# Kernel tuning notes

Hardware: AMD Instinct MI355X
Metric: run time of the kernel (lower is better)

The kernel has to match this reference:

```python
import jax, jax.numpy as jnp
import numpy as np

B, T, S = 4, 16, 4096
H, KV, D, DIM = 32, 8, 128, 4096
BASE = 10000.0
START = 2048
SCALE = 1.0 / np.sqrt(D)


def _rope(t, cos, sin):
    # t: [B, T, nh, D]; ggml 'normal' rope rotates adjacent pairs (x[2i], x[2i+1])
    b, tt, nh, d = t.shape
    t2 = t.reshape(b, tt, nh, d // 2, 2)
    x0, x1 = t2[..., 0], t2[..., 1]
    c = cos[None, :, None, :]  # [1, T, 1, D/2]
    s = sin[None, :, None, :]
    r = jnp.stack([x0 * c - x1 * s, x0 * s + x1 * c], axis=-1)
    return r.reshape(b, tt, nh, d)


def setup_inputs() -> dict:
    key = jax.random.key(0)
    ks = jax.random.split(key, 8)
    x = jax.random.normal(ks[0], (B, T, DIM), dtype=jnp.float32)
    k_cache = jax.random.normal(ks[1], (B, S, KV, D), dtype=jnp.float32)
    v_cache = jax.random.normal(ks[2], (B, S, KV, D), dtype=jnp.float32)
    wq = jax.random.normal(ks[3], (H * D, DIM), dtype=jnp.float32) * 0.02
    wk = jax.random.normal(ks[4], (KV * D, DIM), dtype=jnp.float32) * 0.02
    wv = jax.random.normal(ks[5], (KV * D, DIM), dtype=jnp.float32) * 0.02
    wo = jax.random.normal(ks[6], (DIM, H * D), dtype=jnp.float32) * 0.02
    input_pos = jnp.arange(T, dtype=jnp.int32) + START  # contiguous decode chunk
    inv_freq = BASE ** (-jnp.arange(0, D, 2, dtype=jnp.float32) / D)  # [D/2]
    ang = input_pos.astype(jnp.float32)[:, None] * inv_freq[None, :]  # [T, D/2]
    freqs_cos = jnp.cos(ang)
    freqs_sin = jnp.sin(ang)
    # causal mask: kv position <= query absolute position, [T, S] bool
    attn_mask = jnp.arange(S, dtype=jnp.int32)[None, :] <= input_pos[:, None]
    return {"x": x, "freqs_cos": freqs_cos, "freqs_sin": freqs_sin,
            "input_pos": input_pos, "attn_mask": attn_mask,
            "k_cache": k_cache, "v_cache": v_cache,
            "wq": wq, "wk": wk, "wv": wv, "wo": wo}


def reference(x, freqs_cos, freqs_sin, input_pos, attn_mask, k_cache, v_cache, wq, wk, wv, wo):
    b, t, _ = x.shape
    q = (x @ wq.T).reshape(b, t, H, D)
    k = (x @ wk.T).reshape(b, t, KV, D)
    v = (x @ wv.T).reshape(b, t, KV, D)
    q = _rope(q, freqs_cos, freqs_sin)
    k = _rope(k, freqs_cos, freqs_sin)
    # KV-cache scatter (index_copy_ along dim 1)
    kc = k_cache.at[:, input_pos].set(k)  # [B, S, KV, D]
    vc = v_cache.at[:, input_pos].set(v)
    g = H // KV
    qh = q.transpose(0, 2, 1, 3).reshape(b, KV, g, t, D)  # [B, KV, g, T, D]
    kf = kc.transpose(0, 2, 1, 3)  # [B, KV, S, D]
    vf = vc.transpose(0, 2, 1, 3)
    scores = jnp.einsum('bkgtd,bksd->bkgts', qh, kf) * SCALE
    scores = jnp.where(attn_mask[None, None, None], scores, jnp.finfo(scores.dtype).min)
    probs = jax.nn.softmax(scores, axis=-1)
    y = jnp.einsum('bkgts,bksd->bkgtd', probs, vf)  # [B, KV, g, T, D]
    y = y.reshape(b, H, t, D).transpose(0, 2, 1, 3).reshape(b, t, H * D)
    return y @ wo.T
```

## Files before the change

kernel.cpp:

```cpp
#include <hip/hip_runtime.h>
#include <hip/hip_bf16.h>


#define SCALE_F 0.08838834764831845f

typedef __attribute__((ext_vector_type(8))) short bf16x8;
typedef __attribute__((ext_vector_type(4))) float f32x4;

__device__ __forceinline__ unsigned short f2b(float f) {
    __hip_bfloat16 h = __float2bfloat16(f);
    return *reinterpret_cast<unsigned short*>(&h);
}

__device__ __forceinline__ bf16x8 pack8(float4 a, float4 b) {
    bf16x8 r;
    r[0] = (short)f2b(a.x); r[1] = (short)f2b(a.y); r[2] = (short)f2b(a.z); r[3] = (short)f2b(a.w);
    r[4] = (short)f2b(b.x); r[5] = (short)f2b(b.y); r[6] = (short)f2b(b.z); r[7] = (short)f2b(b.w);
    return r;
}

__device__ __forceinline__ void gl_lds16(const void* g, void* l) {
    __builtin_amdgcn_global_load_lds(
        (const __attribute__((address_space(1))) void*)g,
        (__attribute__((address_space(3))) void*)l, 16, 0, 0);
}


__global__ __launch_bounds__(256) void xcvt_kernel(
    const float* __restrict__ x, unsigned short* __restrict__ xb)
{
    const int flat = blockIdx.x * 256 + threadIdx.x;
    const int m = flat >> 9, rem = flat & 511;
    const int c = rem >> 2, j = rem & 3;
    const float* src = x + (size_t)m * 4096 + c * 32 + j * 8;
    float4 a = *(const float4*)src, b = *(const float4*)(src + 4);
    *(bf16x8*)(xb + c * 2048 + m * 32 + ((j ^ (m & 3)) * 8)) = pack8(a, b);
}

#define GEMM_BODY(WPTR, NN, LDW, APTR, CG_BASE, NCHUNK, ACC)                                   \
    const int l15 = lane & 15, lh = lane >> 4;                                                 \
    const int wr8 = lane >> 3, wc8 = lane & 7;                                                 \
    const float* wsrc = (WPTR) + (size_t)((NN) + 8 * wid + wr8) * (LDW)                        \
                      + ((wc8 ^ (wr8 & 7)) * 4);                                               \
    const unsigned short* asrc = (APTR) + (size_t)(CG_BASE) * 2048 + wid * 512 + lane * 8;     \
    float* wdst = &wlds[0][0] + wid * 256;                                \
    unsigned short* adst = &alds[0][0] + wid * 512;                     \
    _Pragma("unroll")                                                                          \
    for (int pc = 0; pc < 2; ++pc) {                                                           \
        gl_lds16(wsrc + (size_t)pc * 32, wdst + (size_t)pc * 1024);                            \
        gl_lds16(asrc + (size_t)pc * 2048, adst + (size_t)pc * 2048);                          \
    }                                                                                          \
    const int key = l15 & 7;                                                                   \
    const int akey = (l15 & 3);                                                                \
    for (int c = 0; c < (NCHUNK); ++c) {                                                       \
        if (c + 2 < (NCHUNK)) {                                                                \
            const int bq = (c + 2) & 3;                                                        \
            gl_lds16(wsrc + (size_t)(c + 2) * 32, wdst + (size_t)bq * 1024);                   \
            gl_lds16(asrc + (size_t)(c + 2) * 2048, adst + (size_t)bq * 2048);                 \
        }                                                                                      \
        if (c + 2 < (NCHUNK))      asm volatile("s_waitcnt vmcnt(4)" ::: "memory");            \
        else if (c + 1 < (NCHUNK)) asm volatile("s_waitcnt vmcnt(2)" ::: "memory");            \
        else                       asm volatile("s_waitcnt vmcnt(0)" ::: "memory");            \
        __builtin_amdgcn_s_barrier();                                                          \
        const int buf = c & 3;                                                                 \
        const float* wt = &wlds[buf][0];                                                       \
        const unsigned short* at = &alds[buf][0];                                              \
        const int arow = 16 * wid + l15;                                                       \
        bf16x8 a = *(const bf16x8*)(at + arow * 32 + ((lh ^ akey) * 8));                       \
        const float* w0p = wt + l15 * 32;                                                      \
        const float* w1p = wt + (16 + l15) * 32;                                               \
        const int c0 = ((2 * lh) ^ key) * 4, c1 = ((2 * lh + 1) ^ key) * 4;                    \
        bf16x8 b0 = pack8(*(const float4*)(w0p + c0), *(const float4*)(w0p + c1));             \
        bf16x8 b1 = pack8(*(const float4*)(w1p + c0), *(const float4*)(w1p + c1));             \
        ACC[0] = __builtin_amdgcn_mfma_f32_16x16x32_bf16(a, b0, ACC[0], 0, 0, 0);              \
        ACC[1] = __builtin_amdgcn_mfma_f32_16x16x32_bf16(a, b1, ACC[1], 0, 0, 0);              \
        __builtin_amdgcn_s_barrier();                                                          \
    }

__global__ __launch_bounds__(256) void qkv_gemm_kernel(
    const unsigned short* __restrict__ xb,
    const float* __restrict__ wq, const float* __restrict__ wk, const float* __restrict__ wvp,
    float* __restrict__ part)
{
    __shared__ float wlds[4][1024];
    __shared__ unsigned short alds[4][2048];
    const int tid = threadIdx.x, lane = tid & 63, wid = tid >> 6;
    const int n0 = blockIdx.x * 32;
    const int split = blockIdx.y;

    const float* wptr; int nn;
    if (n0 < 4096)      { wptr = wq;  nn = n0; }
    else if (n0 < 5120) { wptr = wk;  nn = n0 - 4096; }
    else                { wptr = wvp; nn = n0 - 5120; }

    f32x4 acc[2];
    acc[0] = (f32x4){0.f,0.f,0.f,0.f};
    acc[1] = (f32x4){0.f,0.f,0.f,0.f};

    const float* wbase = wptr + split * 512;
    GEMM_BODY(wbase, nn, 4096, xb, split * 16, 16, acc)

    float* pp = part + (size_t)split * 64 * 6144 + n0;
    #pragma unroll
    for (int nh = 0; nh < 2; ++nh)
        #pragma unroll
        for (int r = 0; r < 4; ++r)
            pp[(16 * wid + 4 * (lane >> 4) + r) * 6144 + nh * 16 + (lane & 15)] = acc[nh][r];
}

__global__ __launch_bounds__(256) void qkv_reduce_kernel(
    const float* __restrict__ part,
    const float* __restrict__ fcos, const float* __restrict__ fsin,
    unsigned short* __restrict__ q_out, unsigned short* __restrict__ k_new,
    unsigned short* __restrict__ v_new)
{
    const int gid = blockIdx.x * 256 + threadIdx.x;
    const int m = gid / 1536;
    const int n = (gid % 1536) * 4;
    float4 s = {0.f,0.f,0.f,0.f};
    #pragma unroll
    for (int sp = 0; sp < 8; ++sp) {
        float4 v = *(const float4*)(part + (size_t)(sp * 64 + m) * 6144 + n);
        s.x += v.x; s.y += v.y; s.z += v.z; s.w += v.w;
    }
    const int t = m & 15, b = m >> 4;
    ushort4 o;
    if (n < 5120) {
        int d = n & 127;
        float c0 = fcos[t * 64 + (d >> 1)],     s0 = fsin[t * 64 + (d >> 1)];
        float c1 = fcos[t * 64 + (d >> 1) + 1], s1 = fsin[t * 64 + (d >> 1) + 1];
        o.x = f2b(s.x * c0 - s.y * s0);
        o.y = f2b(s.x * s0 + s.y * c0);
        o.z = f2b(s.z * c1 - s.w * s1);
        o.w = f2b(s.z * s1 + s.w * c1);
    } else {
        o.x = f2b(s.x); o.y = f2b(s.y); o.z = f2b(s.z); o.w = f2b(s.w);
    }
    if (n < 4096) {
        int h = n >> 7, d = n & 127;
        int row = (b * 8 + (h >> 2)) * 64 + (h & 3) * 16 + t;
        *(ushort4*)(q_out + row * 128 + d) = o;
    } else if (n < 5120) {
        int idx = n - 4096, kvh = idx >> 7, d = idx & 127;
        *(ushort4*)(k_new + ((b * 8 + kvh) * 16 + t) * 128 + d) = o;
    } else {
        int idx = n - 5120, kvh = idx >> 7, d = idx & 127;
        *(ushort4*)(v_new + ((b * 8 + kvh) * 16 + t) * 128 + d) = o;
    }
}

__global__ __launch_bounds__(256) void attn_kernel(
    const float* __restrict__ k_cache, const float* __restrict__ v_cache,
    const unsigned short* __restrict__ q_glob,
    const unsigned short* __restrict__ k_new, const unsigned short* __restrict__ v_new,
    float* __restrict__ y_part, float* __restrict__ ml)
{
    __shared__ unsigned short smem[32256];
    unsigned short* kv_lds = smem;
    unsigned short* p_lds  = smem + 21504;

    const int bk = blockIdx.x >> 4;
    const int c  = blockIdx.x & 15;
    const int b = bk >> 3, kvh = bk & 7;
    const int tid = threadIdx.x, lane = tid & 63, wid = tid >> 6;
    const int s0 = c * 128;
    const bool last = (c == 15);

    bf16x8 aq[4];
    {
        const unsigned short* qp = q_glob + (bk * 64 + 16 * wid + (lane & 15)) * 128 + 8 * (lane >> 4);
        #pragma unroll
        for (int kk = 0; kk < 4; ++kk) aq[kk] = *(const bf16x8*)(qp + kk * 32);
    }

    const int rr = tid >> 5, ln4 = (tid & 31) * 4;
    {
        const float* kb = k_cache + ((size_t)(b * 4096 + s0) * 8 + kvh) * 128;
        #pragma unroll 4
        for (int it = 0; it < 16; ++it) {
            int srow = it * 8 + rr;
            float4 kf = *(const float4*)(kb + (size_t)srow * 1024 + ln4);
            ushort4 k4; k4.x = f2b(kf.x); k4.y = f2b(kf.y); k4.z = f2b(kf.z); k4.w = f2b(kf.w);
            *(ushort4*)&kv_lds[srow * 136 + ln4] = k4;
        }
        if (last) {
            int row = tid >> 4, c8 = (tid & 15) * 8;
            *(bf16x8*)&kv_lds[(128 + row) * 136 + c8] =
                *(const bf16x8*)(k_new + (bk * 16 + row) * 128 + c8);
        }
    }
    __syncthreads();

    f32x4 sc[9];
    f32x4 zero4 = {0.f,0.f,0.f,0.f};
    #pragma unroll
    for (int st = 0; st < 9; ++st) sc[st] = zero4;
    #pragma unroll
    for (int kk = 0; kk < 4; ++kk) {
        #pragma unroll
        for (int st = 0; st < 9; ++st) {
            if (st == 8 && !last) continue;
            bf16x8 bf = *(bf16x8*)&kv_lds[(st * 16 + (lane & 15)) * 136 + kk * 32 + 8 * (lane >> 4)];
            sc[st] = __builtin_amdgcn_mfma_f32_16x16x32_bf16(aq[kk], bf, sc[st], 0, 0, 0);
        }
    }

    float mrow[4], lrow[4];
    #pragma unroll
    for (int r = 0; r < 4; ++r) {
        int trow = 4 * (lane >> 4) + r;
        float mx = -3.0e38f;
        #pragma unroll
        for (int st = 0; st < 9; ++st) {
            if (st == 8 && !last) continue;
            float s = sc[st][r] * SCALE_F;
            if (st == 8 && (lane & 15) > trow) s = -3.0e38f;
            sc[st][r] = s;
            mx = fmaxf(mx, s);
        }
        mx = fmaxf(mx, __shfl_xor(mx, 1));
        mx = fmaxf(mx, __shfl_xor(mx, 2));
        mx = fmaxf(mx, __shfl_xor(mx, 4));
        mx = fmaxf(mx, __shfl_xor(mx, 8));
        float sum = 0.f;
        #pragma unroll
        for (int st = 0; st < 9; ++st) {
            if (st == 8 && !last) continue;
            float p = __expf(sc[st][r] - mx);
            sc[st][r] = p;
            sum += p;
        }
        sum += __shfl_xor(sum, 1);
        sum += __shfl_xor(sum, 2);
        sum += __shfl_xor(sum, 4);
        sum += __shfl_xor(sum, 8);
        mrow[r] = mx; lrow[r] = sum;
    }

    #pragma unroll
    for (int st = 0; st < 9; ++st) {
        if (st == 8 && !last) continue;
        #pragma unroll
        for (int r = 0; r < 4; ++r)
            p_lds[(16 * wid + 4 * (lane >> 4) + r) * 168 + st * 16 + (lane & 15)] = f2b(sc[st][r]);
    }
    if ((lane & 15) == 0) {
        #pragma unroll
        for (int r = 0; r < 4; ++r) {
            int row = 16 * wid + 4 * (lane >> 4) + r;
            ml[(bk * 16 + c) * 128 + row * 2 + 0] = mrow[r];
            ml[(bk * 16 + c) * 128 + row * 2 + 1] = lrow[r];
        }
    }
    __syncthreads();

    {
        const float* vb = v_cache + ((size_t)(b * 4096 + s0) * 8 + kvh) * 128;
        #pragma unroll 4
        for (int it = 0; it < 16; ++it) {
            int srow = it * 8 + rr;
            float4 vf = *(const float4*)(vb + (size_t)srow * 1024 + ln4);
            kv_lds[(ln4 + 0) * 168 + srow] = f2b(vf.x);
            kv_lds[(ln4 + 1) * 168 + srow] = f2b(vf.y);
            kv_lds[(ln4 + 2) * 168 + srow] = f2b(vf.z);
            kv_lds[(ln4 + 3) * 168 + srow] = f2b(vf.w);
        }
        if (last) {
            int row = tid >> 4, c8 = (tid & 15) * 8;
            bf16x8 vv = *(const bf16x8*)(v_new + (bk * 16 + row) * 128 + c8);
            #pragma unroll
            for (int u = 0; u < 8; ++u)
                kv_lds[(c8 + u) * 168 + 128 + row] = (unsigned short)vv[u];
            int pr = tid >> 2, pc = (tid & 3) * 4;
            #pragma unroll
            for (int u = 0; u < 4; ++u) p_lds[pr * 168 + 144 + pc + u] = 0;
            int vr = tid >> 1, vc = (tid & 1) * 8;
            #pragma unroll
            for (int u = 0; u < 8; ++u) kv_lds[vr * 168 + 144 + vc + u] = 0;
        }
    }
    __syncthreads();

    f32x4 o_[8];
    #pragma unroll
    for (int nt = 0; nt < 8; ++nt) o_[nt] = zero4;
    #pragma unroll
    for (int ks = 0; ks < 5; ++ks) {
        if (ks == 4 && !last) continue;
        bf16x8 a = *(bf16x8*)&p_lds[(16 * wid + (lane & 15)) * 168 + ks * 32 + 8 * (lane >> 4)];
        #pragma unroll
        for (int nt = 0; nt < 8; ++nt) {
            bf16x8 bf = *(bf16x8*)&kv_lds[(nt * 16 + (lane & 15)) * 168 + ks * 32 + 8 * (lane >> 4)];
            o_[nt] = __builtin_amdgcn_mfma_f32_16x16x32_bf16(a, bf, o_[nt], 0, 0, 0);
        }
    }
    float* yp = y_part + (size_t)(bk * 16 + c) * 8192;
    #pragma unroll
    for (int nt = 0; nt < 8; ++nt) {
        #pragma unroll
        for (int r = 0; r < 4; ++r)
            yp[(16 * wid + 4 * (lane >> 4) + r) * 128 + nt * 16 + (lane & 15)] = o_[nt][r];
    }
}

__global__ __launch_bounds__(256) void combine_kernel(
    const float* __restrict__ y_part, const float* __restrict__ ml,
    unsigned short* __restrict__ y_attn)
{
    const int bid = blockIdx.x;
    const int bk = bid >> 3, rg = bid & 7;
    const int b = bk >> 3, kvh = bk & 7;
    const int tid = threadIdx.x;
    const int d = tid & 127, r2 = tid >> 7;
    for (int rr = 0; rr < 8; rr += 2) {
        int row = rg * 8 + rr + r2;
        float mv[16], lv[16], M = -3.0e38f;
        #pragma unroll
        for (int cc = 0; cc < 16; ++cc) {
            mv[cc] = ml[(bk * 16 + cc) * 128 + row * 2 + 0];
            lv[cc] = ml[(bk * 16 + cc) * 128 + row * 2 + 1];
            M = fmaxf(M, mv[cc]);
        }
        float den = 0.f, acc = 0.f;
        #pragma unroll
        for (int cc = 0; cc < 16; ++cc) {
            float co = __expf(mv[cc] - M);
            den += co * lv[cc];
            acc += co * y_part[((size_t)(bk * 16 + cc) * 64 + row) * 128 + d];
        }
        float y = acc / den;
        int gi = row >> 4, t = row & 15;
        int m = b * 16 + t;
        int n = (kvh * 4 + gi) * 128 + d;
        int c = n >> 5, j = (n >> 3) & 3, lo = n & 7;
        y_attn[c * 2048 + m * 32 + ((j ^ (m & 3)) * 8) + lo] = f2b(y);
    }
}

__global__ __launch_bounds__(256) void proj_gemm_kernel(
    const unsigned short* __restrict__ y_attn, const float* __restrict__ wo,
    float* __restrict__ part)
{
    __shared__ float wlds[4][1024];
    __shared__ unsigned short alds[4][2048];
    const int tid = threadIdx.x, lane = tid & 63, wid = tid >> 6;
    const int n0 = blockIdx.x * 32;
    const int split = blockIdx.y;

    f32x4 acc[2];
    acc[0] = (f32x4){0.f,0.f,0.f,0.f};
    acc[1] = (f32x4){0.f,0.f,0.f,0.f};

    const float* wbase = wo + split * 512;
    GEMM_BODY(wbase, n0, 4096, y_attn, split * 16, 16, acc)

    float* pp = part + (size_t)split * 64 * 4096 + n0;
    #pragma unroll
    for (int nh = 0; nh < 2; ++nh)
        #pragma unroll
        for (int r = 0; r < 4; ++r)
            pp[(16 * wid + 4 * (lane >> 4) + r) * 4096 + nh * 16 + (lane & 15)] = acc[nh][r];
}

__global__ __launch_bounds__(256) void proj_reduce_kernel(
    const float* __restrict__ part, float* __restrict__ out)
{
    const int gid = blockIdx.x * 256 + threadIdx.x;
    const int m = gid >> 10;
    const int n = (gid & 1023) * 4;
    float4 s = {0.f,0.f,0.f,0.f};
    #pragma unroll
    for (int sp = 0; sp < 8; ++sp) {
        float4 v = *(const float4*)(part + (size_t)(sp * 64 + m) * 4096 + n);
        s.x += v.x; s.y += v.y; s.z += v.z; s.w += v.w;
    }
    *(float4*)(out + (size_t)m * 4096 + n) = s;
}

extern "C" void kernel_launch(void* const* d_in, const int* in_sizes, int n_in,
                              void* d_out, int out_size, void* d_ws, size_t ws_size,
                              hipStream_t stream)
{
    const float* x       = (const float*)d_in[0];
    const float* fcos    = (const float*)d_in[1];
    const float* fsin    = (const float*)d_in[2];
    const float* k_cache = (const float*)d_in[5];
    const float* v_cache = (const float*)d_in[6];
    const float* wq      = (const float*)d_in[7];
    const float* wk      = (const float*)d_in[8];
    const float* wv      = (const float*)d_in[9];
    const float* wo      = (const float*)d_in[10];

    char* p = (char*)d_ws;
    unsigned short* q_out  = (unsigned short*)p; p += 4 * 8 * 64 * 128 * 2;
    unsigned short* k_new  = (unsigned short*)p; p += 4 * 8 * 16 * 128 * 2;
    unsigned short* v_new  = (unsigned short*)p; p += 4 * 8 * 16 * 128 * 2;
    unsigned short* y_attn = (unsigned short*)p; p += 64 * 4096 * 2;
    unsigned short* x_bf16 = (unsigned short*)p; p += 64 * 4096 * 2;
    float* mlbuf  = (float*)p; p += 32 * 16 * 64 * 2 * 4;
    float* y_part = (float*)p; p += (size_t)32 * 16 * 64 * 128 * 4;
    float* bigbuf = (float*)p;

    xcvt_kernel<<<128, 256, 0, stream>>>(x, x_bf16);
    qkv_gemm_kernel<<<dim3(192, 8), 256, 0, stream>>>(x_bf16, wq, wk, wv, bigbuf);
    qkv_reduce_kernel<<<384, 256, 0, stream>>>(bigbuf, fcos, fsin, q_out, k_new, v_new);
    attn_kernel<<<512, 256, 0, stream>>>(k_cache, v_cache, q_out, k_new, v_new, y_part, mlbuf);
    combine_kernel<<<256, 256, 0, stream>>>(y_part, mlbuf, y_attn);
    proj_gemm_kernel<<<dim3(128, 8), 256, 0, stream>>>(y_attn, wo, bigbuf);
    proj_reduce_kernel<<<256, 256, 0, stream>>>(bigbuf, (float*)d_out);
}
```

Baseline: 85.65 us.

## Retile QKV and output GEMMs to 256-wide N tiles with 16-way split-K

Both weight GEMMs now give each block a 256-column N tile, with each wave computing a 64x64 register tile (4x4 MFMA fragments) instead of a 32-column tile. The K dimension is split 16 ways rather than 8, and the reduce kernels sum 16 partials. Pipelining drops from four buffers to double buffering with larger chunks. The aim is to reuse each loaded A fragment across more MFMAs and cut per-block overhead, at the cost of far fewer blocks (384 and 256), more partial-sum traffic, and higher register and LDS use.

```diff
diff --git a/kernel.cpp b/kernel.cpp
--- a/kernel.cpp
+++ b/kernel.cpp
@@ -37,43 +37,43 @@
     *(bf16x8*)(xb + c * 2048 + m * 32 + ((j ^ (m & 3)) * 8)) = pack8(a, b);
 }
 
-#define GEMM_BODY(WPTR, NN, LDW, APTR, CG_BASE, NCHUNK, ACC)                                   \
+#define GEMM_TILE(WLANE, ASRC, NC, ACC)                                                        \
     const int l15 = lane & 15, lh = lane >> 4;                                                 \
-    const int wr8 = lane >> 3, wc8 = lane & 7;                                                 \
-    const float* wsrc = (WPTR) + (size_t)((NN) + 8 * wid + wr8) * (LDW)                        \
-                      + ((wc8 ^ (wr8 & 7)) * 4);                                               \
-    const unsigned short* asrc = (APTR) + (size_t)(CG_BASE) * 2048 + wid * 512 + lane * 8;     \
-    float* wdst = &wlds[0][0] + wid * 256;                                \
-    unsigned short* adst = &alds[0][0] + wid * 512;                     \
+    float* wd0 = &wlds[0][0] + wid * 2048;                                                     \
+    unsigned short* ad0 = &alds[0][0] + wid * 512;                                             \
     _Pragma("unroll")                                                                          \
-    for (int pc = 0; pc < 2; ++pc) {                                                           \
-        gl_lds16(wsrc + (size_t)pc * 32, wdst + (size_t)pc * 1024);                            \
-        gl_lds16(asrc + (size_t)pc * 2048, adst + (size_t)pc * 2048);                          \
-    }                                                                                          \
-    const int key = l15 & 7;                                                                   \
-    const int akey = (l15 & 3);                                                                \
-    for (int c = 0; c < (NCHUNK); ++c) {                                                       \
-        if (c + 2 < (NCHUNK)) {                                                                \
-            const int bq = (c + 2) & 3;                                                        \
-            gl_lds16(wsrc + (size_t)(c + 2) * 32, wdst + (size_t)bq * 1024);                   \
-            gl_lds16(asrc + (size_t)(c + 2) * 2048, adst + (size_t)bq * 2048);                 \
+    for (int i = 0; i < 8; ++i) gl_lds16((WLANE) + (size_t)i * 8 * 4096, wd0 + i * 256);       \
+    gl_lds16((ASRC), ad0);                                                                     \
+    for (int c = 0; c < (NC); ++c) {                                                           \
+        if (c + 1 < (NC)) {                                                                    \
+            const int bq = (c + 1) & 1;                                                        \
+            float* wd = &wlds[0][0] + bq * 8192 + wid * 2048;                                  \
+            unsigned short* ad = &alds[0][0] + bq * 2048 + wid * 512;                          \
+            _Pragma("unroll")                                                                  \
+            for (int i = 0; i < 8; ++i)                                                        \
+                gl_lds16((WLANE) + (size_t)i * 8 * 4096 + (c + 1) * 32, wd + i * 256);         \
+            gl_lds16((ASRC) + (size_t)(c + 1) * 2048, ad);                                     \
+            asm volatile("s_waitcnt vmcnt(9)" ::: "memory");                                   \
+        } else {                                                                               \
+            asm volatile("s_waitcnt vmcnt(0)" ::: "memory");                                   \
         }                                                                                      \
-        if (c + 2 < (NCHUNK))      asm volatile("s_waitcnt vmcnt(4)" ::: "memory");            \
-        else if (c + 1 < (NCHUNK)) asm volatile("s_waitcnt vmcnt(2)" ::: "memory");            \
-        else                       asm volatile("s_waitcnt vmcnt(0)" ::: "memory");            \
         __builtin_amdgcn_s_barrier();                                                          \
-        const int buf = c & 3;                                                                 \
-        const float* wt = &wlds[buf][0];                                                       \
-        const unsigned short* at = &alds[buf][0];                                              \
-        const int arow = 16 * wid + l15;                                                       \
-        bf16x8 a = *(const bf16x8*)(at + arow * 32 + ((lh ^ akey) * 8));                       \
-        const float* w0p = wt + l15 * 32;                                                      \
-        const float* w1p = wt + (16 + l15) * 32;                                               \
-        const int c0 = ((2 * lh) ^ key) * 4, c1 = ((2 * lh + 1) ^ key) * 4;                    \
-        bf16x8 b0 = pack8(*(const float4*)(w0p + c0), *(const float4*)(w0p + c1));             \
-        bf16x8 b1 = pack8(*(const float4*)(w1p + c0), *(const float4*)(w1p + c1));             \
-        ACC[0] = __builtin_amdgcn_mfma_f32_16x16x32_bf16(a, b0, ACC[0], 0, 0, 0);              \
-        ACC[1] = __builtin_amdgcn_mfma_f32_16x16x32_bf16(a, b1, ACC[1], 0, 0, 0);              \
+        const int buf = c & 1;                                                                 \
+        const unsigned short* at = &alds[0][0] + buf * 2048;                                   \
+        const float* wt = &wlds[0][0] + buf * 8192;                                            \
+        bf16x8 afr[4];                                                                         \
+        _Pragma("unroll")                                                                      \
+        for (int m = 0; m < 4; ++m)                                                            \
+            afr[m] = *(const bf16x8*)(at + (16 * m + l15) * 32 + ((lh ^ (l15 & 3)) * 8));      \
+        const int c0 = ((2 * lh) ^ (l15 & 7)) * 4, c1 = ((2 * lh + 1) ^ (l15 & 7)) * 4;        \
+        _Pragma("unroll")                                                                      \
+        for (int nf = 0; nf < 4; ++nf) {                                                       \
+            const float* wr = wt + (wid * 64 + nf * 16 + l15) * 32;                            \
+            bf16x8 b = pack8(*(const float4*)(wr + c0), *(const float4*)(wr + c1));            \
+            _Pragma("unroll")                                                                  \
+            for (int m = 0; m < 4; ++m)                                                        \
+                ACC[m][nf] = __builtin_amdgcn_mfma_f32_16x16x32_bf16(afr[m], b, ACC[m][nf], 0, 0, 0); \
+        }                                                                                      \
         __builtin_amdgcn_s_barrier();                                                          \
     }
 
@@ -82,30 +82,38 @@
     const float* __restrict__ wq, const float* __restrict__ wk, const float* __restrict__ wvp,
     float* __restrict__ part)
 {
-    __shared__ float wlds[4][1024];
-    __shared__ unsigned short alds[4][2048];
+    __shared__ float wlds[2][8192];
+    __shared__ unsigned short alds[2][2048];
     const int tid = threadIdx.x, lane = tid & 63, wid = tid >> 6;
-    const int n0 = blockIdx.x * 32;
+    const int n0 = blockIdx.x * 256;
     const int split = blockIdx.y;
+    const int kbase = split * 256;
 
     const float* wptr; int nn;
     if (n0 < 4096)      { wptr = wq;  nn = n0; }
     else if (n0 < 5120) { wptr = wk;  nn = n0 - 4096; }
     else                { wptr = wvp; nn = n0 - 5120; }
 
-    f32x4 acc[2];
-    acc[0] = (f32x4){0.f,0.f,0.f,0.f};
-    acc[1] = (f32x4){0.f,0.f,0.f,0.f};
-
-    const float* wbase = wptr + split * 512;
-    GEMM_BODY(wbase, nn, 4096, xb, split * 16, 16, acc)
-
-    float* pp = part + (size_t)split * 64 * 6144 + n0;
-    #pragma unroll
-    for (int nh = 0; nh < 2; ++nh)
-        #pragma unroll
-        for (int r = 0; r < 4; ++r)
-            pp[(16 * wid + 4 * (lane >> 4) + r) * 6144 + nh * 16 + (lane & 15)] = acc[nh][r];
+    const float* wlane = wptr + (size_t)(nn + wid * 64 + (lane >> 3)) * 4096 + kbase
+                       + (((lane & 7) ^ ((lane >> 3) & 7)) * 4);
+    const unsigned short* asrc = xb + (size_t)(split * 8) * 2048 + wid * 512 + lane * 8;
+
+    f32x4 acc[4][4];
+    #pragma unroll
+    for (int m = 0; m < 4; ++m)
+        #pragma unroll
+        for (int nf = 0; nf < 4; ++nf) acc[m][nf] = (f32x4){0.f,0.f,0.f,0.f};
+
+    GEMM_TILE(wlane, asrc, 8, acc)
+
+    float* pp = part + (size_t)split * 64 * 6144 + n0 + wid * 64;
+    #pragma unroll
+    for (int m = 0; m < 4; ++m)
+        #pragma unroll
+        for (int nf = 0; nf < 4; ++nf)
+            #pragma unroll
+            for (int r = 0; r < 4; ++r)
+                pp[(16 * m + 4 * lh + r) * 6144 + nf * 16 + l15] = acc[m][nf][r];
 }
 
 __global__ __launch_bounds__(256) void qkv_reduce_kernel(
@@ -119,7 +127,7 @@
     const int n = (gid % 1536) * 4;
     float4 s = {0.f,0.f,0.f,0.f};
     #pragma unroll
-    for (int sp = 0; sp < 8; ++sp) {
+    for (int sp = 0; sp < 16; ++sp) {
         float4 v = *(const float4*)(part + (size_t)(sp * 64 + m) * 6144 + n);
         s.x += v.x; s.y += v.y; s.z += v.z; s.w += v.w;
     }
@@ -341,25 +349,33 @@
     const unsigned short* __restrict__ y_attn, const float* __restrict__ wo,
     float* __restrict__ part)
 {
-    __shared__ float wlds[4][1024];
-    __shared__ unsigned short alds[4][2048];
+    __shared__ float wlds[2][8192];
+    __shared__ unsigned short alds[2][2048];
     const int tid = threadIdx.x, lane = tid & 63, wid = tid >> 6;
-    const int n0 = blockIdx.x * 32;
+    const int n0 = blockIdx.x * 256;
     const int split = blockIdx.y;
-
-    f32x4 acc[2];
-    acc[0] = (f32x4){0.f,0.f,0.f,0.f};
-    acc[1] = (f32x4){0.f,0.f,0.f,0.f};
-
-    const float* wbase = wo + split * 512;
-    GEMM_BODY(wbase, n0, 4096, y_attn, split * 16, 16, acc)
-
-    float* pp = part + (size_t)split * 64 * 4096 + n0;
-    #pragma unroll
-    for (int nh = 0; nh < 2; ++nh)
-        #pragma unroll
-        for (int r = 0; r < 4; ++r)
-            pp[(16 * wid + 4 * (lane >> 4) + r) * 4096 + nh * 16 + (lane & 15)] = acc[nh][r];
+    const int kbase = split * 256;
+
+    const float* wlane = wo + (size_t)(n0 + wid * 64 + (lane >> 3)) * 4096 + kbase
+                       + (((lane & 7) ^ ((lane >> 3) & 7)) * 4);
+    const unsigned short* asrc = y_attn + (size_t)(split * 8) * 2048 + wid * 512 + lane * 8;
+
+    f32x4 acc[4][4];
+    #pragma unroll
+    for (int m = 0; m < 4; ++m)
+        #pragma unroll
+        for (int nf = 0; nf < 4; ++nf) acc[m][nf] = (f32x4){0.f,0.f,0.f,0.f};
+
+    GEMM_TILE(wlane, asrc, 8, acc)
+
+    float* pp = part + (size_t)split * 64 * 4096 + n0 + wid * 64;
+    #pragma unroll
+    for (int m = 0; m < 4; ++m)
+        #pragma unroll
+        for (int nf = 0; nf < 4; ++nf)
+            #pragma unroll
+            for (int r = 0; r < 4; ++r)
+                pp[(16 * m + 4 * lh + r) * 4096 + nf * 16 + l15] = acc[m][nf][r];
 }
 
 __global__ __launch_bounds__(256) void proj_reduce_kernel(
@@ -370,7 +386,7 @@
     const int n = (gid & 1023) * 4;
     float4 s = {0.f,0.f,0.f,0.f};
     #pragma unroll
-    for (int sp = 0; sp < 8; ++sp) {
+    for (int sp = 0; sp < 16; ++sp) {
         float4 v = *(const float4*)(part + (size_t)(sp * 64 + m) * 4096 + n);
         s.x += v.x; s.y += v.y; s.z += v.z; s.w += v.w;
     }
@@ -402,10 +418,10 @@
     float* bigbuf = (float*)p;
 
     xcvt_kernel<<<128, 256, 0, stream>>>(x, x_bf16);
-    qkv_gemm_kernel<<<dim3(192, 8), 256, 0, stream>>>(x_bf16, wq, wk, wv, bigbuf);
+    qkv_gemm_kernel<<<dim3(24, 16), 256, 0, stream>>>(x_bf16, wq, wk, wv, bigbuf);
     qkv_reduce_kernel<<<384, 256, 0, stream>>>(bigbuf, fcos, fsin, q_out, k_new, v_new);
     attn_kernel<<<512, 256, 0, stream>>>(k_cache, v_cache, q_out, k_new, v_new, y_part, mlbuf);
     combine_kernel<<<256, 256, 0, stream>>>(y_part, mlbuf, y_attn);
-    proj_gemm_kernel<<<dim3(128, 8), 256, 0, stream>>>(y_attn, wo, bigbuf);
+    proj_gemm_kernel<<<dim3(16, 16), 256, 0, stream>>>(y_attn, wo, bigbuf);
     proj_reduce_kernel<<<256, 256, 0, stream>>>(bigbuf, (float*)d_out);
 }
```

New measurement: 84.85 us. Within noise of the previous version (-0.9%).
